# Performance work log

Measured on AMD Instinct MI355X. Metric: run time of the kernel, lower is better.

Reference implementation:

```python
import jax, jax.numpy as jnp
import numpy as np

B, S, D = 1, 2048, 2048
H, KV = 32, 8
HD = D // H          # 64
R = H // KV          # 4 (GQA repeat factor)
ROPE_BASE = 10000.0


def setup_inputs() -> dict:
    key = jax.random.key(0)
    ks = jax.random.split(key, 5)
    x = jax.random.normal(ks[0], (B, S, D), jnp.float32)
    # Real rotary frequencies as (cos, sin) pairs: [S, HD//2, 2]
    inv_freq = 1.0 / (ROPE_BASE ** (np.arange(0, HD, 2, dtype=np.float64) / HD))
    ang = np.outer(np.arange(S, dtype=np.float64), inv_freq)
    freqs_cis = jnp.asarray(np.stack([np.cos(ang), np.sin(ang)], axis=-1), jnp.float32)
    std = 0.02
    wq = jax.random.normal(ks[1], (H * HD, D), jnp.float32) * std
    wk = jax.random.normal(ks[2], (KV * HD, D), jnp.float32) * std
    wv = jax.random.normal(ks[3], (KV * HD, D), jnp.float32) * std
    wo = jax.random.normal(ks[4], (D, H * HD), jnp.float32) * std
    return {"x": x, "freqs_cis": freqs_cis, "wq": wq, "wk": wk, "wv": wv, "wo": wo}


def _apply_rope(x, cos, sin):
    # x: [b, s, h, hd]; cos/sin: [s, hd//2]. Complex multiply on interleaved pairs.
    xr = x.reshape(*x.shape[:-1], HD // 2, 2)
    x0, x1 = xr[..., 0], xr[..., 1]
    c = cos[None, :, None, :]
    s = sin[None, :, None, :]
    o0 = x0 * c - x1 * s
    o1 = x0 * s + x1 * c
    return jnp.stack([o0, o1], axis=-1).reshape(x.shape)


def reference(x, freqs_cis, wq, wk, wv, wo):
    b, s, _ = x.shape
    q = (x @ wq.T).reshape(b, s, H, HD)
    k = (x @ wk.T).reshape(b, s, KV, HD)
    v = (x @ wv.T).reshape(b, s, KV, HD)
    cos, sin = freqs_cis[..., 0], freqs_cis[..., 1]
    q = _apply_rope(q, cos, sin)
    k = _apply_rope(k, cos, sin)
    # GQA: group q heads instead of repeat_interleave on k/v.
    # repeat_interleave maps kv-head g -> q heads [g*R, (g+1)*R), matching this reshape.
    qg = q.reshape(b, s, KV, R, HD)
    scale = 1.0 / np.sqrt(HD)
    scores = jnp.einsum('bsgrd,btgd->bgrst', qg, k) * scale  # [b, KV, R, s, t]
    causal = jnp.tril(jnp.ones((s, s), dtype=bool))
    scores = jnp.where(causal, scores, jnp.float32(-1e9))
    attn = jax.nn.softmax(scores.astype(jnp.float32), axis=-1).astype(q.dtype)
    out = jnp.einsum('bgrst,btgd->bsgrd', attn, v).reshape(b, s, H * HD)
    return out @ wo.T
```

## Files before the change

### kernel.cpp

```cpp
#include <hip/hip_runtime.h>

typedef unsigned short u16;
typedef unsigned int u32;
typedef __bf16 bf16x8 __attribute__((ext_vector_type(8)));
typedef unsigned short ushort8 __attribute__((ext_vector_type(8)));
typedef float floatx4 __attribute__((ext_vector_type(4)));
typedef u32 u32x2 __attribute__((ext_vector_type(2)));

#define S_LEN 2048
#define NH 32
#define NKV 8
#define HD_ 64
#define LDQ 3072

__device__ __forceinline__ u16 f2bf(float f) {
  unsigned u = __builtin_bit_cast(unsigned, f);
  u += 0x7FFF + ((u >> 16) & 1);
  return (u16)(u >> 16);
}
__device__ __forceinline__ float bf2f(u16 h) {
  unsigned u = ((unsigned)h) << 16;
  return __builtin_bit_cast(float, u);
}
__device__ __forceinline__ bf16x8 ld8(const u16* p) {
  return __builtin_bit_cast(bf16x8, *(const ushort8*)p);
}
__device__ __forceinline__ floatx4 mfma16(bf16x8 a, bf16x8 b, floatx4 c) {
  return __builtin_amdgcn_mfma_f32_16x16x32_bf16(a, b, c, 0, 0, 0);
}
__device__ __forceinline__ u32 pk2bf(float a, float b) {
  u32 ua = __builtin_bit_cast(u32, a) + 0x8000u;
  u32 ub = __builtin_bit_cast(u32, b) + 0x8000u;
  return __builtin_amdgcn_perm(ub, ua, 0x07060302);
}

__global__ void cvt_kernel(const float* __restrict__ in, u16* __restrict__ out, int n4) {
  int i = blockIdx.x * blockDim.x + threadIdx.x;
  if (i >= n4) return;
  float4 v = ((const float4*)in)[i];
  ((ushort4*)out)[i] = make_ushort4(f2bf(v.x), f2bf(v.y), f2bf(v.z), f2bf(v.w));
}

template <int TM, int TN, int OUT_BF16>
__global__ __launch_bounds__(256) void gemm_db(
    const u16* __restrict__ A, const u16* __restrict__ B, void* __restrict__ C,
    int ldc, int K, int lda) {
  __shared__ __align__(16) u16 As[2][TM * 64];
  __shared__ __align__(16) u16 Bs[2][TN * 64];
  const int tid = threadIdx.x;
  const int wave = tid >> 6, lane = tid & 63;
  const int quad = lane >> 4, l16 = lane & 15;
  const int bm = blockIdx.y * TM, bn = blockIdx.x * TN;
  const int wr = (wave >> 1) * (TM / 2), wc = (wave & 1) * (TN / 2);
  constexpr int MI = TM / 32, NI = TN / 32;
  const int crow = tid >> 3, col8 = tid & 7;

  size_t aoff[MI], boff[NI];
#pragma unroll
  for (int j = 0; j < MI; j++) aoff[j] = (size_t)(bm + crow + j * 32) * lda + col8 * 8;
#pragma unroll
  for (int j = 0; j < NI; j++) boff[j] = (size_t)(bn + crow + j * 32) * K + col8 * 8;

  ushort8 a8[MI], b8[NI];
  auto load_tiles = [&](int k0) {
#pragma unroll
    for (int j = 0; j < MI; j++) a8[j] = *(const ushort8*)(A + aoff[j] + k0);
#pragma unroll
    for (int j = 0; j < NI; j++) b8[j] = *(const ushort8*)(B + boff[j] + k0);
  };
  auto write_tiles = [&](int p) {
#pragma unroll
    for (int j = 0; j < MI; j++) {
      const int row = crow + j * 32;
      *(ushort8*)&As[p][row * 64 + ((col8 ^ (row & 7)) * 8)] = a8[j];
    }
#pragma unroll
    for (int j = 0; j < NI; j++) {
      const int row = crow + j * 32;
      *(ushort8*)&Bs[p][row * 64 + ((col8 ^ (row & 7)) * 8)] = b8[j];
    }
  };

  floatx4 acc[MI][NI] = {};
  load_tiles(0);
  write_tiles(0);
  __syncthreads();
  int p = 0;
  for (int k0 = 0; k0 < K; k0 += 64) {
    const bool more = (k0 + 64 < K);
    if (more) load_tiles(k0 + 64);
#pragma unroll
    for (int kh = 0; kh < 2; kh++) {
      bf16x8 af[MI], bfr[NI];
#pragma unroll
      for (int mi = 0; mi < MI; mi++) {
        const int row = wr + mi * 16 + l16;
        af[mi] = ld8(&As[p][row * 64 + (((kh * 4 + quad) ^ (row & 7)) * 8)]);
      }
#pragma unroll
      for (int ni = 0; ni < NI; ni++) {
        const int row = wc + ni * 16 + l16;
        bfr[ni] = ld8(&Bs[p][row * 64 + (((kh * 4 + quad) ^ (row & 7)) * 8)]);
      }
#pragma unroll
      for (int mi = 0; mi < MI; mi++)
#pragma unroll
        for (int ni = 0; ni < NI; ni++)
          acc[mi][ni] = mfma16(af[mi], bfr[ni], acc[mi][ni]);
    }
    if (more) {
      write_tiles(p ^ 1);
      __syncthreads();
      p ^= 1;
    }
  }

#pragma unroll
  for (int mi = 0; mi < MI; mi++)
#pragma unroll
    for (int ni = 0; ni < NI; ni++)
#pragma unroll
      for (int r = 0; r < 4; r++) {
        const int row = bm + wr + mi * 16 + quad * 4 + r;
        const int col = bn + wc + ni * 16 + l16;
        if (OUT_BF16) ((u16*)C)[(size_t)row * ldc + col] = f2bf(acc[mi][ni][r]);
        else          ((float*)C)[(size_t)row * ldc + col] = acc[mi][ni][r];
      }
}

__global__ void rope_kernel(u16* __restrict__ qk, const float* __restrict__ fc, int h_bits,
                            int row_stride, float scale) {
  int idx = blockIdx.x * blockDim.x + threadIdx.x;
  int d = idx & 31;
  int t = idx >> 5;
  int hh = t & ((1 << h_bits) - 1);
  int s = t >> h_bits;
  float c  = fc[s * 64 + d * 2];
  float sn = fc[s * 64 + d * 2 + 1];
  size_t base = (size_t)s * row_stride + hh * 64 + d * 2;
  float x0 = bf2f(qk[base]), x1 = bf2f(qk[base + 1]);
  qk[base]     = f2bf((x0 * c - x1 * sn) * scale);
  qk[base + 1] = f2bf((x0 * sn + x1 * c) * scale);
}

__global__ void transpose_v(const u16* __restrict__ qkv, u16* __restrict__ vT) {
  int idx = blockIdx.x * blockDim.x + threadIdx.x;
  int s = idx & (S_LEN - 1);
  int t = idx >> 11;
  vT[idx] = qkv[(size_t)s * LDQ + 2560 + t];
}

__global__ __launch_bounds__(256) void attn_kernel(const u16* qkv, const u16* __restrict__ vT,
                                                   u16* __restrict__ o) {
  __shared__ __align__(16) u16 Ks[2][64 * 64];
  __shared__ __align__(16) u16 Vs[2][64 * 64];
  __shared__ __align__(16) u16 pS[8][16 * 64];
  const int h = blockIdx.x;
  const int g = h >> 2;
  const int tid = threadIdx.x;
  const int wave = tid >> 6, lane = tid & 63;
  const int quad = lane >> 4, l16 = lane & 15;
  const int y = (int)blockIdx.y;
  const int p_ = (y < 8) ? y : 23 - y;
  const int qlo = p_, qhi = 31 - p_;

  const ushort8 ones_u = {0x3F80, 0x3F80, 0x3F80, 0x3F80, 0x3F80, 0x3F80, 0x3F80, 0x3F80};
  const bf16x8 onesA = __builtin_bit_cast(bf16x8, ones_u);

  const int qrow = wave * 16 + l16;
  const int qgA = qlo * 64 + qrow, qgB = qhi * 64 + qrow;
  const size_t qoffA = (size_t)qgA * LDQ + h * HD_;
  const size_t qoffB = (size_t)qgB * LDQ + h * HD_;
  bf16x8 qfA0 = ld8(qkv + qoffA + quad * 8);
  bf16x8 qfA1 = ld8(qkv + qoffA + 32 + quad * 8);
  bf16x8 qfB0 = ld8(qkv + qoffB + quad * 8);
  bf16x8 qfB1 = ld8(qkv + qoffB + 32 + quad * 8);

  const int r0 = tid >> 3, r1 = r0 + 32;
  const int col8 = tid & 7;
  const int so = (col8 ^ (r0 & 7)) * 8;
  const int o0 = col8 * 8;
  const u16* ksrc = qkv + 2048 + g * HD_;
  const u16* vsrc = vT + (size_t)g * HD_ * S_LEN;

  ushort8 kp0 = *(const ushort8*)(ksrc + (size_t)r0 * LDQ + o0);
  ushort8 kp1 = *(const ushort8*)(ksrc + (size_t)r1 * LDQ + o0);
  ushort8 vp0 = *(const ushort8*)(vsrc + (size_t)r0 * S_LEN + o0);
  ushort8 vp1 = *(const ushort8*)(vsrc + (size_t)r1 * S_LEN + o0);

  floatx4 OA[4] = {}, OB[4] = {};
  floatx4 lA = {}, lB = {};
  u16* myPA = &pS[wave][0];
  u16* myPB = &pS[wave + 4][0];

  *(ushort8*)&Ks[0][r0 * 64 + so] = kp0;
  *(ushort8*)&Ks[0][r1 * 64 + so] = kp1;
  *(ushort8*)&Vs[0][r0 * 64 + so] = vp0;
  *(ushort8*)&Vs[0][r1 * 64 + so] = vp1;
  kp0 = *(const ushort8*)(ksrc + (size_t)(64 + r0) * LDQ + o0);
  kp1 = *(const ushort8*)(ksrc + (size_t)(64 + r1) * LDQ + o0);
  vp0 = *(const ushort8*)(vsrc + (size_t)r0 * S_LEN + 64 + o0);
  vp1 = *(const ushort8*)(vsrc + (size_t)r1 * S_LEN + 64 + o0);
  __syncthreads();
  int pp = 0;

  for (int kt = 0; kt <= qhi; kt++) {
    const int kbase = kt * 64;
    const bool more = kt < qhi;
    if (more) {
      *(ushort8*)&Ks[pp ^ 1][r0 * 64 + so] = kp0;
      *(ushort8*)&Ks[pp ^ 1][r1 * 64 + so] = kp1;
      *(ushort8*)&Vs[pp ^ 1][r0 * 64 + so] = vp0;
      *(ushort8*)&Vs[pp ^ 1][r1 * 64 + so] = vp1;
      if (kt + 1 < qhi) {
        const int nb = kbase + 128;
        kp0 = *(const ushort8*)(ksrc + (size_t)(nb + r0) * LDQ + o0);
        kp1 = *(const ushort8*)(ksrc + (size_t)(nb + r1) * LDQ + o0);
        vp0 = *(const ushort8*)(vsrc + (size_t)r0 * S_LEN + nb + o0);
        vp1 = *(const ushort8*)(vsrc + (size_t)r1 * S_LEN + nb + o0);
      }
    }
    const u16* Kc = &Ks[pp][0];
    const u16* Vc = &Vs[pp][0];
    const bool actA = (kt <= qlo);

    floatx4 sfA[4], sfB[4];
#pragma unroll
    for (int sub = 0; sub < 4; sub++) {
      const int row = sub * 16 + l16;
      const u16* kb = Kc + row * 64;
      bf16x8 k0 = ld8(kb + ((quad ^ (l16 & 7)) * 8));
      bf16x8 k1 = ld8(kb + (((4 + quad) ^ (l16 & 7)) * 8));
      floatx4 sB = {};
      sB = mfma16(k0, qfB0, sB);
      sB = mfma16(k1, qfB1, sB);
      sfB[sub] = sB;
      if (actA) {
        floatx4 sA = {};
        sA = mfma16(k0, qfA0, sA);
        sA = mfma16(k1, qfA1, sA);
        sfA[sub] = sA;
      }
    }
    if (kt == qhi) {
#pragma unroll
      for (int sub = 0; sub < 4; sub++)
#pragma unroll
        for (int r = 0; r < 4; r++)
          if (kbase + sub * 16 + quad * 4 + r > qgB) sfB[sub][r] = -INFINITY;
    }
    if (kt == qlo) {
#pragma unroll
      for (int sub = 0; sub < 4; sub++)
#pragma unroll
        for (int r = 0; r < 4; r++)
          if (kbase + sub * 16 + quad * 4 + r > qgA) sfA[sub][r] = -INFINITY;
    }

    u32x2 pkA[4], pkB[4];
#pragma unroll
    for (int sub = 0; sub < 4; sub++) {
      pkB[sub].x = pk2bf(__builtin_amdgcn_exp2f(sfB[sub][0]), __builtin_amdgcn_exp2f(sfB[sub][1]));
      pkB[sub].y = pk2bf(__builtin_amdgcn_exp2f(sfB[sub][2]), __builtin_amdgcn_exp2f(sfB[sub][3]));
      if (actA) {
        pkA[sub].x = pk2bf(__builtin_amdgcn_exp2f(sfA[sub][0]), __builtin_amdgcn_exp2f(sfA[sub][1]));
        pkA[sub].y = pk2bf(__builtin_amdgcn_exp2f(sfA[sub][2]), __builtin_amdgcn_exp2f(sfA[sub][3]));
      }
    }

    bf16x8 vf[4][2];
#pragma unroll
    for (int nt = 0; nt < 4; nt++) {
      const u16* vb = Vc + (nt * 16 + l16) * 64;
      vf[nt][0] = ld8(vb + ((quad ^ (l16 & 7)) * 8));
      vf[nt][1] = ld8(vb + (((4 + quad) ^ (l16 & 7)) * 8));
    }

#pragma unroll
    for (int sub = 0; sub < 4; sub++) {
      const int slot = (2 * sub + (quad >> 1)) ^ (l16 & 7);
      const int a = l16 * 64 + slot * 8 + (quad & 1) * 4;
      *(u32x2*)&myPB[a] = pkB[sub];
      if (actA) *(u32x2*)&myPA[a] = pkA[sub];
    }
    asm volatile("s_waitcnt lgkmcnt(0)" ::: "memory");
    bf16x8 pB0 = ld8(&myPB[l16 * 64 + ((quad ^ (l16 & 7)) * 8)]);
    bf16x8 pB1 = ld8(&myPB[l16 * 64 + (((4 + quad) ^ (l16 & 7)) * 8)]);
#pragma unroll
    for (int nt = 0; nt < 4; nt++) {
      OB[nt] = mfma16(vf[nt][0], pB0, OB[nt]);
      OB[nt] = mfma16(vf[nt][1], pB1, OB[nt]);
    }
    lB = mfma16(onesA, pB0, lB);
    lB = mfma16(onesA, pB1, lB);
    if (actA) {
      bf16x8 pA0 = ld8(&myPA[l16 * 64 + ((quad ^ (l16 & 7)) * 8)]);
      bf16x8 pA1 = ld8(&myPA[l16 * 64 + (((4 + quad) ^ (l16 & 7)) * 8)]);
#pragma unroll
      for (int nt = 0; nt < 4; nt++) {
        OA[nt] = mfma16(vf[nt][0], pA0, OA[nt]);
        OA[nt] = mfma16(vf[nt][1], pA1, OA[nt]);
      }
      lA = mfma16(onesA, pA0, lA);
      lA = mfma16(onesA, pA1, lA);
    }
    if (more) {
      __syncthreads();
      pp ^= 1;
    }
  }

  const float invA = 1.0f / lA[0];
  const float invB = 1.0f / lB[0];
  const size_t ooffA = (size_t)qgA * 2048 + h * HD_;
  const size_t ooffB = (size_t)qgB * 2048 + h * HD_;
#pragma unroll
  for (int nt = 0; nt < 4; nt++)
#pragma unroll
    for (int r = 0; r < 4; r++) {
      const int hd = nt * 16 + quad * 4 + r;
      o[ooffA + hd] = f2bf(OA[nt][r] * invA);
      o[ooffB + hd] = f2bf(OB[nt][r] * invB);
    }
}

extern "C" void kernel_launch(void* const* d_in, const int* in_sizes, int n_in,
                              void* d_out, int out_size, void* d_ws, size_t ws_size,
                              hipStream_t stream) {
  const float* x  = (const float*)d_in[0];
  const float* fc = (const float*)d_in[1];
  const float* wq = (const float*)d_in[2];
  const float* wk = (const float*)d_in[3];
  const float* wv = (const float*)d_in[4];
  const float* wo = (const float*)d_in[5];
  float* out = (float*)d_out;

  char* ws = (char*)d_ws;
  const size_t MB = 1024 * 1024;
  u16* qkv = (u16*)(ws);
  u16* wb  = (u16*)(ws + 12 * MB);
  u16* vTb = (u16*)(ws + 12 * MB);
  u16* wob = (u16*)(ws + 14 * MB);
  u16* ob  = (u16*)(ws + 22 * MB);
  u16* xb  = (u16*)d_out;
  (void)ws_size; (void)n_in; (void)in_sizes; (void)out_size;

  cvt_kernel<<<4096, 256, 0, stream>>>(x,  xb, 1048576);
  cvt_kernel<<<4096, 256, 0, stream>>>(wq, wb, 1048576);
  cvt_kernel<<<1024, 256, 0, stream>>>(wk, wb + (size_t)2048 * 2048, 262144);
  cvt_kernel<<<1024, 256, 0, stream>>>(wv, wb + (size_t)2560 * 2048, 262144);
  gemm_db<128, 96, 1><<<dim3(32, 16), 256, 0, stream>>>(xb, wb, qkv, LDQ, 2048, 2048);
  cvt_kernel<<<4096, 256, 0, stream>>>(wo, wob, 1048576);
  rope_kernel<<<8192, 256, 0, stream>>>(qkv, fc, 5, LDQ, 0.18033688f);
  rope_kernel<<<2048, 256, 0, stream>>>(qkv + 2048, fc, 3, LDQ, 1.0f);
  transpose_v<<<4096, 256, 0, stream>>>(qkv, vTb);
  attn_kernel<<<dim3(NH, 16), 256, 0, stream>>>(qkv, vTb, ob);
  gemm_db<128, 64, 0><<<dim3(32, 16), 256, 0, stream>>>(ob, wob, out, 2048, 2048, 2048);
}
```

Measured before the change: 231.8 us.

## Serialize paired query tiles in attention and retune GEMM tile shapes

The attention kernel stops processing both paired query tiles (A and B) together on every key tile. It now walks 33 key tiles in sequence, first the A tile's causal range and then the B tile's, with a single P scratch buffer per wave. The aim is a uniform loop body with no actA branching and lower register and LDS pressure, at the cost of loading K/V tiles up to the A range twice. The QKV and output GEMMs switch to smaller tiles with more blocks, which should improve occupancy and load balance on the many compute units.

```diff
diff --git a/kernel.cpp b/kernel.cpp
--- a/kernel.cpp
+++ b/kernel.cpp
@@ -154,21 +154,20 @@
                                                    u16* __restrict__ o) {
   __shared__ __align__(16) u16 Ks[2][64 * 64];
   __shared__ __align__(16) u16 Vs[2][64 * 64];
-  __shared__ __align__(16) u16 pS[8][16 * 64];
+  __shared__ __align__(16) u16 pS[4][16 * 64];
   const int h = blockIdx.x;
   const int g = h >> 2;
   const int tid = threadIdx.x;
   const int wave = tid >> 6, lane = tid & 63;
   const int quad = lane >> 4, l16 = lane & 15;
-  const int y = (int)blockIdx.y;
-  const int p_ = (y < 8) ? y : 23 - y;
-  const int qlo = p_, qhi = 31 - p_;
+  const int p_ = (int)blockIdx.y;
+  const int qtB = 31 - p_;
 
   const ushort8 ones_u = {0x3F80, 0x3F80, 0x3F80, 0x3F80, 0x3F80, 0x3F80, 0x3F80, 0x3F80};
   const bf16x8 onesA = __builtin_bit_cast(bf16x8, ones_u);
 
   const int qrow = wave * 16 + l16;
-  const int qgA = qlo * 64 + qrow, qgB = qhi * 64 + qrow;
+  const int qgA = p_ * 64 + qrow, qgB = qtB * 64 + qrow;
   const size_t qoffA = (size_t)qgA * LDQ + h * HD_;
   const size_t qoffB = (size_t)qgB * LDQ + h * HD_;
   bf16x8 qfA0 = ld8(qkv + qoffA + quad * 8);
@@ -183,127 +182,112 @@
   const u16* ksrc = qkv + 2048 + g * HD_;
   const u16* vsrc = vT + (size_t)g * HD_ * S_LEN;
 
-  ushort8 kp0 = *(const ushort8*)(ksrc + (size_t)r0 * LDQ + o0);
-  ushort8 kp1 = *(const ushort8*)(ksrc + (size_t)r1 * LDQ + o0);
-  ushort8 vp0 = *(const ushort8*)(vsrc + (size_t)r0 * S_LEN + o0);
-  ushort8 vp1 = *(const ushort8*)(vsrc + (size_t)r1 * S_LEN + o0);
+  ushort8 kp0, kp1, vp0, vp1;
+  auto gload = [&](int t) {
+    const int tb = t * 64;
+    kp0 = *(const ushort8*)(ksrc + (size_t)(tb + r0) * LDQ + o0);
+    kp1 = *(const ushort8*)(ksrc + (size_t)(tb + r1) * LDQ + o0);
+    vp0 = *(const ushort8*)(vsrc + (size_t)r0 * S_LEN + tb + o0);
+    vp1 = *(const ushort8*)(vsrc + (size_t)r1 * S_LEN + tb + o0);
+  };
+  auto tile_of = [&](int i) { return (i <= p_) ? i : (i - p_ - 1); };
 
   floatx4 OA[4] = {}, OB[4] = {};
   floatx4 lA = {}, lB = {};
-  u16* myPA = &pS[wave][0];
-  u16* myPB = &pS[wave + 4][0];
-
+  u16* myP = &pS[wave][0];
+
+  gload(0);
   *(ushort8*)&Ks[0][r0 * 64 + so] = kp0;
   *(ushort8*)&Ks[0][r1 * 64 + so] = kp1;
   *(ushort8*)&Vs[0][r0 * 64 + so] = vp0;
   *(ushort8*)&Vs[0][r1 * 64 + so] = vp1;
-  kp0 = *(const ushort8*)(ksrc + (size_t)(64 + r0) * LDQ + o0);
-  kp1 = *(const ushort8*)(ksrc + (size_t)(64 + r1) * LDQ + o0);
-  vp0 = *(const ushort8*)(vsrc + (size_t)r0 * S_LEN + 64 + o0);
-  vp1 = *(const ushort8*)(vsrc + (size_t)r1 * S_LEN + 64 + o0);
+  gload(tile_of(1));
   __syncthreads();
   int pp = 0;
 
-  for (int kt = 0; kt <= qhi; kt++) {
+  for (int i = 0; i < 33; i++) {
+    const bool more = (i < 32);
+    const bool isA = (i <= p_);
+    const int kt = isA ? i : (i - p_ - 1);
     const int kbase = kt * 64;
-    const bool more = kt < qhi;
+    const int qg = isA ? qgA : qgB;
+    const bf16x8 q0 = isA ? qfA0 : qfB0;
+    const bf16x8 q1 = isA ? qfA1 : qfB1;
+
+    const u16* Kc = &Ks[pp][0];
+    const u16* Vc = &Vs[pp][0];
+    bf16x8 kf[4][2], vf[4][2];
+#pragma unroll
+    for (int sub = 0; sub < 4; sub++) {
+      const u16* kb = Kc + (sub * 16 + l16) * 64;
+      kf[sub][0] = ld8(kb + ((quad ^ (l16 & 7)) * 8));
+      kf[sub][1] = ld8(kb + (((4 + quad) ^ (l16 & 7)) * 8));
+    }
+#pragma unroll
+    for (int nt = 0; nt < 4; nt++) {
+      const u16* vb = Vc + (nt * 16 + l16) * 64;
+      vf[nt][0] = ld8(vb + ((quad ^ (l16 & 7)) * 8));
+      vf[nt][1] = ld8(vb + (((4 + quad) ^ (l16 & 7)) * 8));
+    }
+
     if (more) {
       *(ushort8*)&Ks[pp ^ 1][r0 * 64 + so] = kp0;
       *(ushort8*)&Ks[pp ^ 1][r1 * 64 + so] = kp1;
       *(ushort8*)&Vs[pp ^ 1][r0 * 64 + so] = vp0;
       *(ushort8*)&Vs[pp ^ 1][r1 * 64 + so] = vp1;
-      if (kt + 1 < qhi) {
-        const int nb = kbase + 128;
-        kp0 = *(const ushort8*)(ksrc + (size_t)(nb + r0) * LDQ + o0);
-        kp1 = *(const ushort8*)(ksrc + (size_t)(nb + r1) * LDQ + o0);
-        vp0 = *(const ushort8*)(vsrc + (size_t)r0 * S_LEN + nb + o0);
-        vp1 = *(const ushort8*)(vsrc + (size_t)r1 * S_LEN + nb + o0);
-      }
-    }
-    const u16* Kc = &Ks[pp][0];
-    const u16* Vc = &Vs[pp][0];
-    const bool actA = (kt <= qlo);
-
-    floatx4 sfA[4], sfB[4];
+      if (i < 31) gload(tile_of(i + 2));
+    }
+
+    floatx4 sf[4];
 #pragma unroll
     for (int sub = 0; sub < 4; sub++) {
-      const int row = sub * 16 + l16;
-      const u16* kb = Kc + row * 64;
-      bf16x8 k0 = ld8(kb + ((quad ^ (l16 & 7)) * 8));
-      bf16x8 k1 = ld8(kb + (((4 + quad) ^ (l16 & 7)) * 8));
-      floatx4 sB = {};
-      sB = mfma16(k0, qfB0, sB);
-      sB = mfma16(k1, qfB1, sB);
-      sfB[sub] = sB;
-      if (actA) {
-        floatx4 sA = {};
-        sA = mfma16(k0, qfA0, sA);
-        sA = mfma16(k1, qfA1, sA);
-        sfA[sub] = sA;
-      }
-    }
-    if (kt == qhi) {
+      floatx4 s = {};
+      s = mfma16(kf[sub][0], q0, s);
+      s = mfma16(kf[sub][1], q1, s);
+      sf[sub] = s;
+    }
+    if (i == p_ || i == 32) {
 #pragma unroll
       for (int sub = 0; sub < 4; sub++)
 #pragma unroll
         for (int r = 0; r < 4; r++)
-          if (kbase + sub * 16 + quad * 4 + r > qgB) sfB[sub][r] = -INFINITY;
-    }
-    if (kt == qlo) {
-#pragma unroll
-      for (int sub = 0; sub < 4; sub++)
-#pragma unroll
-        for (int r = 0; r < 4; r++)
-          if (kbase + sub * 16 + quad * 4 + r > qgA) sfA[sub][r] = -INFINITY;
-    }
-
-    u32x2 pkA[4], pkB[4];
+          if (kbase + sub * 16 + quad * 4 + r > qg) sf[sub][r] = -INFINITY;
+    }
+
+    u32x2 pk[4];
 #pragma unroll
     for (int sub = 0; sub < 4; sub++) {
-      pkB[sub].x = pk2bf(__builtin_amdgcn_exp2f(sfB[sub][0]), __builtin_amdgcn_exp2f(sfB[sub][1]));
-      pkB[sub].y = pk2bf(__builtin_amdgcn_exp2f(sfB[sub][2]), __builtin_amdgcn_exp2f(sfB[sub][3]));
-      if (actA) {
-        pkA[sub].x = pk2bf(__builtin_amdgcn_exp2f(sfA[sub][0]), __builtin_amdgcn_exp2f(sfA[sub][1]));
-        pkA[sub].y = pk2bf(__builtin_amdgcn_exp2f(sfA[sub][2]), __builtin_amdgcn_exp2f(sfA[sub][3]));
-      }
-    }
-
-    bf16x8 vf[4][2];
-#pragma unroll
-    for (int nt = 0; nt < 4; nt++) {
-      const u16* vb = Vc + (nt * 16 + l16) * 64;
-      vf[nt][0] = ld8(vb + ((quad ^ (l16 & 7)) * 8));
-      vf[nt][1] = ld8(vb + (((4 + quad) ^ (l16 & 7)) * 8));
+      pk[sub].x = pk2bf(__builtin_amdgcn_exp2f(sf[sub][0]), __builtin_amdgcn_exp2f(sf[sub][1]));
+      pk[sub].y = pk2bf(__builtin_amdgcn_exp2f(sf[sub][2]), __builtin_amdgcn_exp2f(sf[sub][3]));
     }
 
 #pragma unroll
     for (int sub = 0; sub < 4; sub++) {
       const int slot = (2 * sub + (quad >> 1)) ^ (l16 & 7);
-      const int a = l16 * 64 + slot * 8 + (quad & 1) * 4;
-      *(u32x2*)&myPB[a] = pkB[sub];
-      if (actA) *(u32x2*)&myPA[a] = pkA[sub];
+      *(u32x2*)&myP[l16 * 64 + slot * 8 + (quad & 1) * 4] = pk[sub];
     }
     asm volatile("s_waitcnt lgkmcnt(0)" ::: "memory");
-    bf16x8 pB0 = ld8(&myPB[l16 * 64 + ((quad ^ (l16 & 7)) * 8)]);
-    bf16x8 pB1 = ld8(&myPB[l16 * 64 + (((4 + quad) ^ (l16 & 7)) * 8)]);
-#pragma unroll
-    for (int nt = 0; nt < 4; nt++) {
-      OB[nt] = mfma16(vf[nt][0], pB0, OB[nt]);
-      OB[nt] = mfma16(vf[nt][1], pB1, OB[nt]);
-    }
-    lB = mfma16(onesA, pB0, lB);
-    lB = mfma16(onesA, pB1, lB);
-    if (actA) {
-      bf16x8 pA0 = ld8(&myPA[l16 * 64 + ((quad ^ (l16 & 7)) * 8)]);
-      bf16x8 pA1 = ld8(&myPA[l16 * 64 + (((4 + quad) ^ (l16 & 7)) * 8)]);
+    bf16x8 pf0 = ld8(&myP[l16 * 64 + ((quad ^ (l16 & 7)) * 8)]);
+    bf16x8 pf1 = ld8(&myP[l16 * 64 + (((4 + quad) ^ (l16 & 7)) * 8)]);
+
+    if (isA) {
 #pragma unroll
       for (int nt = 0; nt < 4; nt++) {
-        OA[nt] = mfma16(vf[nt][0], pA0, OA[nt]);
-        OA[nt] = mfma16(vf[nt][1], pA1, OA[nt]);
-      }
-      lA = mfma16(onesA, pA0, lA);
-      lA = mfma16(onesA, pA1, lA);
-    }
+        OA[nt] = mfma16(vf[nt][0], pf0, OA[nt]);
+        OA[nt] = mfma16(vf[nt][1], pf1, OA[nt]);
+      }
+      lA = mfma16(onesA, pf0, lA);
+      lA = mfma16(onesA, pf1, lA);
+    } else {
+#pragma unroll
+      for (int nt = 0; nt < 4; nt++) {
+        OB[nt] = mfma16(vf[nt][0], pf0, OB[nt]);
+        OB[nt] = mfma16(vf[nt][1], pf1, OB[nt]);
+      }
+      lB = mfma16(onesA, pf0, lB);
+      lB = mfma16(onesA, pf1, lB);
+    }
+
     if (more) {
       __syncthreads();
       pp ^= 1;
@@ -349,11 +333,11 @@
   cvt_kernel<<<4096, 256, 0, stream>>>(wq, wb, 1048576);
   cvt_kernel<<<1024, 256, 0, stream>>>(wk, wb + (size_t)2048 * 2048, 262144);
   cvt_kernel<<<1024, 256, 0, stream>>>(wv, wb + (size_t)2560 * 2048, 262144);
-  gemm_db<128, 96, 1><<<dim3(32, 16), 256, 0, stream>>>(xb, wb, qkv, LDQ, 2048, 2048);
+  gemm_db<128, 64, 1><<<dim3(48, 16), 256, 0, stream>>>(xb, wb, qkv, LDQ, 2048, 2048);
   cvt_kernel<<<4096, 256, 0, stream>>>(wo, wob, 1048576);
   rope_kernel<<<8192, 256, 0, stream>>>(qkv, fc, 5, LDQ, 0.18033688f);
   rope_kernel<<<2048, 256, 0, stream>>>(qkv + 2048, fc, 3, LDQ, 1.0f);
   transpose_v<<<4096, 256, 0, stream>>>(qkv, vTb);
   attn_kernel<<<dim3(NH, 16), 256, 0, stream>>>(qkv, vTb, ob);
-  gemm_db<128, 64, 0><<<dim3(32, 16), 256, 0, stream>>>(ob, wob, out, 2048, 2048, 2048);
-}
+  gemm_db<64, 64, 0><<<dim3(32, 32), 256, 0, stream>>>(ob, wob, out, 2048, 2048, 2048);
+}
```

Measured after the change: 245.3 us. +5.8%, slower.
